# Kernel optimization log

Measured on AMD Instinct MI355X. Metric: run time of the kernel, lower is better.

Reference implementation:

```python
import jax, jax.numpy as jnp
import numpy as np

N, E, D_IN, HID = 100000, 3200000, 256, 128
EPS = 1e-5  # BatchNorm1d default eps


def batchnorm(x, gamma, beta):
    # training-mode BatchNorm1d: batch stats, biased variance
    mu = x.mean(axis=0)
    var = ((x - mu) ** 2).mean(axis=0)
    return (x - mu) * jax.lax.rsqrt(var + EPS) * gamma + beta


def setup_inputs() -> dict:
    key = jax.random.key(0)
    ks = jax.random.split(key, 6)
    s_in = 1.0 / np.sqrt(D_IN)
    s_h = 1.0 / np.sqrt(HID)
    return {
        "x": jax.random.normal(ks[0], (N, D_IN), jnp.float32),
        "edge_index": jax.random.randint(ks[1], (2, E), 0, N),
        "W1": jax.random.uniform(ks[2], (D_IN, HID), jnp.float32, -s_in, s_in),
        "b1": jnp.zeros((HID,), jnp.float32),
        "g1": jnp.ones((HID,), jnp.float32),
        "be1": jnp.zeros((HID,), jnp.float32),
        "Wl": jax.random.uniform(ks[3], (HID, HID), jnp.float32, -s_h, s_h),
        "bl": jnp.zeros((HID,), jnp.float32),
        "Wr": jax.random.uniform(ks[4], (HID, HID), jnp.float32, -s_h, s_h),
        "g2": jnp.ones((HID,), jnp.float32),
        "be2": jnp.zeros((HID,), jnp.float32),
    }


def reference(x, edge_index, W1, b1, g1, be1, Wl, bl, Wr, g2, be2):
    # input_linear: Linear -> BatchNorm1d, then ReLU
    feat = jax.nn.relu(batchnorm(x @ W1 + b1, g1, be1))  # [N, HID]

    # SAGEConv: mean-aggregate source features at destinations
    src, dst = edge_index[0], edge_index[1]
    msg_sum = jax.ops.segment_sum(feat[src], dst, num_segments=N)       # [N, HID]
    deg = jax.ops.segment_sum(jnp.ones((E, 1), feat.dtype), dst, num_segments=N)
    mean = msg_sum / jnp.maximum(deg, 1.0)

    # out = lin_l(aggr) + lin_r(x); lin_l has bias, lin_r does not (PyG default)
    out = mean @ Wl + bl + feat @ Wr
    out_feat = batchnorm(out, g2, be2)
    return feat, out_feat
```

## Files before the change

kernel.cpp:

```cpp
#include <hip/hip_runtime.h>

#define NN 100000
#define NE 3200000
#define KD 256
#define HD 128
#define NB 782
#define CAP 4608

typedef __bf16 bf16x8 __attribute__((ext_vector_type(8)));
typedef float  f32x8  __attribute__((ext_vector_type(8)));
typedef float  f32x4  __attribute__((ext_vector_type(4)));
typedef float  f32x2  __attribute__((ext_vector_type(2)));
typedef unsigned u32x2 __attribute__((ext_vector_type(2)));
typedef unsigned u32x4 __attribute__((ext_vector_type(4)));

__device__ __forceinline__ f32x4 mfma16(bf16x8 a, bf16x8 b, f32x4 c) {
  return __builtin_amdgcn_mfma_f32_16x16x32_bf16(a, b, c, 0, 0, 0);
}

__global__ void prep_w(const float* __restrict__ W1, const float* __restrict__ Wl,
                       const float* __restrict__ Wr, __bf16* __restrict__ Bt1,
                       __bf16* __restrict__ Bt2, float* __restrict__ stats,
                       int* __restrict__ bucket_cur) {
  if (blockIdx.x == 0) {
    for (int i = threadIdx.x; i < 1024; i += 256) stats[i] = 0.f;
  } else if (blockIdx.x == 1) {
    for (int i = threadIdx.x; i < NB; i += 256) bucket_cur[i] = i * CAP;
  }
  int c = blockIdx.x;
  int k = threadIdx.x;
  Bt1[c * KD + k] = (__bf16)W1[k * HD + c];
  float w = (k < HD) ? Wl[k * HD + c] : Wr[(k - HD) * HD + c];
  Bt2[c * KD + k] = (__bf16)w;
}

__global__ __launch_bounds__(1024) void b_scatter(const int* __restrict__ src,
                                                  const int* __restrict__ dst,
                                                  int* __restrict__ bucket_cur,
                                                  unsigned* __restrict__ pairs) {
  __shared__ int h[NB];
  __shared__ int cur[NB];
  __shared__ int gbase[NB];
  for (int i = threadIdx.x; i < NB; i += 1024) { h[i] = 0; cur[i] = 0; }
  __syncthreads();
  int base = blockIdx.x * 12500;
  for (int i = threadIdx.x; i < 12500; i += 1024)
    atomicAdd(&h[dst[base + i] >> 7], 1);
  __syncthreads();
  for (int b = threadIdx.x; b < NB; b += 1024) {
    int c = h[b];
    gbase[b] = c ? atomicAdd(&bucket_cur[b], c) : 0;
  }
  __syncthreads();
  for (int i = threadIdx.x; i < 12500; i += 1024) {
    int d = dst[base + i];
    int s = src[base + i];
    int b = d >> 7;
    int r = atomicAdd(&cur[b], 1);
    pairs[gbase[b] + r] = ((unsigned)s << 7) | (unsigned)(d & 127);
  }
}

__global__ __launch_bounds__(256) void b_sort(const int* __restrict__ bucket_cur,
                                              unsigned* __restrict__ pc,
                                              int* __restrict__ row_start,
                                              int* __restrict__ row_cnt) {
  __shared__ unsigned sin[CAP];
  __shared__ unsigned sout[CAP];
  __shared__ int h[128], ex[128];
  int b = blockIdx.x;
  int n0 = b * CAP;
  int cnt = bucket_cur[b] - n0;
  if (cnt > CAP) cnt = CAP;
  if (threadIdx.x < 128) h[threadIdx.x] = 0;
  __syncthreads();
  for (int i = threadIdx.x; i < cnt; i += 256) {
    unsigned v = pc[n0 + i];
    sin[i] = v;
    atomicAdd(&h[v & 127], 1);
  }
  __syncthreads();
  if (threadIdx.x < 128) ex[threadIdx.x] = h[threadIdx.x];
  __syncthreads();
  for (int off = 1; off < 128; off <<= 1) {
    int u = 0;
    if (threadIdx.x < 128 && threadIdx.x >= off) u = ex[threadIdx.x - off];
    __syncthreads();
    if (threadIdx.x < 128) ex[threadIdx.x] += u;
    __syncthreads();
  }
  if (threadIdx.x < 128) {
    int c = h[threadIdx.x];
    int excl = ex[threadIdx.x] - c;
    int node = b * 128 + threadIdx.x;
    if (node < NN) {
      row_start[node] = n0 + excl;
      row_cnt[node] = c;
    }
    h[threadIdx.x] = excl;
  }
  __syncthreads();
  for (int i = threadIdx.x; i < cnt; i += 256) {
    unsigned v = sin[i];
    int r = atomicAdd(&h[v & 127], 1);
    sout[r] = v >> 7;
  }
  __syncthreads();
  for (int i = threadIdx.x; i < cnt; i += 256)
    pc[n0 + i] = sout[i];
}

__global__ __launch_bounds__(256, 4) void gemm_x(const float* __restrict__ A,
                                                 const __bf16* __restrict__ Bt,
                                                 float* __restrict__ C,
                                                 float* __restrict__ sumc,
                                                 float* __restrict__ sqc) {
  __shared__ __bf16 sB[64 * KD];
  __shared__ float lsum[64], lsq[64];
  int tid = threadIdx.x;
  int colbase = (blockIdx.x & 1) * 64;
  int rowtile = blockIdx.x >> 1;
  if (tid < 64) { lsum[tid] = 0.f; lsq[tid] = 0.f; }
  int wave = tid >> 6, lane = tid & 63;
  int q = lane >> 4, m = lane & 15;
  int rowbase = rowtile * 256 + wave * 64;
  const float* pa[4];
#pragma unroll
  for (int g = 0; g < 4; ++g) {
    int r = rowbase + g * 16 + m;
    if (r > NN - 1) r = NN - 1;
    pa[g] = A + (size_t)r * KD + q * 8;
  }
  f32x8 u[4];
#pragma unroll
  for (int g = 0; g < 4; ++g) u[g] = *(const f32x8*)(pa[g]);
  for (int i = tid; i < 64 * KD / 8; i += 256) {
    int r = i >> 5, g = i & 31;
    bf16x8 v = *(const bf16x8*)(Bt + (size_t)(colbase + r) * KD + (g << 3));
    *(bf16x8*)(&sB[r * KD + ((g ^ (r & 7)) << 3)]) = v;
  }
  f32x4 acc[4][4];
  f32x4 z = {0.f, 0.f, 0.f, 0.f};
#pragma unroll
  for (int g = 0; g < 4; ++g)
#pragma unroll
    for (int t = 0; t < 4; ++t) acc[g][t] = z;
  __syncthreads();
#pragma unroll
  for (int k0 = 0; k0 < KD; k0 += 32) {
    bf16x8 a[4];
#pragma unroll
    for (int g = 0; g < 4; ++g) a[g] = __builtin_convertvector(u[g], bf16x8);
    if (k0 + 32 < KD) {
#pragma unroll
      for (int g = 0; g < 4; ++g) u[g] = *(const f32x8*)(pa[g] + k0 + 32);
    }
    int gb = (k0 >> 3) + q;
#pragma unroll
    for (int t = 0; t < 4; ++t) {
      int c = t * 16 + m;
      bf16x8 bb = *(const bf16x8*)(&sB[c * KD + ((gb ^ (c & 7)) << 3)]);
#pragma unroll
      for (int g = 0; g < 4; ++g) acc[g][t] = mfma16(a[g], bb, acc[g][t]);
    }
  }
  float ps[4], pq2[4];
#pragma unroll
  for (int t = 0; t < 4; ++t) { ps[t] = 0.f; pq2[t] = 0.f; }
#pragma unroll
  for (int g = 0; g < 4; ++g)
#pragma unroll
    for (int rg = 0; rg < 4; ++rg) {
      int r = rowbase + g * 16 + q * 4 + rg;
      if (r < NN) {
        float* Cr = C + (size_t)r * HD + colbase + m;
#pragma unroll
        for (int t = 0; t < 4; ++t) {
          float v = acc[g][t][rg];
          Cr[t * 16] = v;
          ps[t] += v;
          pq2[t] += v * v;
        }
      }
    }
#pragma unroll
  for (int t = 0; t < 4; ++t) {
    atomicAdd(&lsum[t * 16 + m], ps[t]);
    atomicAdd(&lsq[t * 16 + m], pq2[t]);
  }
  __syncthreads();
  if (tid < 64) {
    atomicAdd(&sumc[colbase + tid], lsum[tid]);
    atomicAdd(&sqc[colbase + tid], lsq[tid]);
  }
}

__global__ __launch_bounds__(256, 4) void gemm_cat(const __bf16* __restrict__ A0,
                                                   const __bf16* __restrict__ A1,
                                                   const __bf16* __restrict__ Bt,
                                                   float* __restrict__ C,
                                                   float* __restrict__ sumc,
                                                   float* __restrict__ sqc) {
  __shared__ __bf16 sB[64 * KD];
  __shared__ float lsum[64], lsq[64];
  int tid = threadIdx.x;
  int colbase = (blockIdx.x & 1) * 64;
  int rowtile = blockIdx.x >> 1;
  if (tid < 64) { lsum[tid] = 0.f; lsq[tid] = 0.f; }
  int wave = tid >> 6, lane = tid & 63;
  int q = lane >> 4, m = lane & 15;
  int rowbase = rowtile * 256 + wave * 64;
  const __bf16* p0[4];
  const __bf16* p1[4];
#pragma unroll
  for (int g = 0; g < 4; ++g) {
    int r = rowbase + g * 16 + m;
    if (r > NN - 1) r = NN - 1;
    p0[g] = A0 + (size_t)r * HD + q * 8;
    p1[g] = A1 + (size_t)r * HD + q * 8;
  }
  bf16x8 u[4];
#pragma unroll
  for (int g = 0; g < 4; ++g) u[g] = *(const bf16x8*)(p0[g]);
  for (int i = tid; i < 64 * KD / 8; i += 256) {
    int r = i >> 5, g = i & 31;
    bf16x8 v = *(const bf16x8*)(Bt + (size_t)(colbase + r) * KD + (g << 3));
    *(bf16x8*)(&sB[r * KD + ((g ^ (r & 7)) << 3)]) = v;
  }
  f32x4 acc[4][4];
  f32x4 z = {0.f, 0.f, 0.f, 0.f};
#pragma unroll
  for (int g = 0; g < 4; ++g)
#pragma unroll
    for (int t = 0; t < 4; ++t) acc[g][t] = z;
  __syncthreads();
#pragma unroll
  for (int k0 = 0; k0 < KD; k0 += 32) {
    bf16x8 a[4];
#pragma unroll
    for (int g = 0; g < 4; ++g) a[g] = u[g];
    int kn = k0 + 32;
    if (kn < KD) {
      int kk = kn & (HD - 1);
#pragma unroll
      for (int g = 0; g < 4; ++g)
        u[g] = (kn < HD) ? *(const bf16x8*)(p0[g] + kk)
                         : *(const bf16x8*)(p1[g] + kk);
    }
    int gb = (k0 >> 3) + q;
#pragma unroll
    for (int t = 0; t < 4; ++t) {
      int c = t * 16 + m;
      bf16x8 bb = *(const bf16x8*)(&sB[c * KD + ((gb ^ (c & 7)) << 3)]);
#pragma unroll
      for (int g = 0; g < 4; ++g) acc[g][t] = mfma16(a[g], bb, acc[g][t]);
    }
  }
  float ps[4], pq2[4];
#pragma unroll
  for (int t = 0; t < 4; ++t) { ps[t] = 0.f; pq2[t] = 0.f; }
#pragma unroll
  for (int g = 0; g < 4; ++g)
#pragma unroll
    for (int rg = 0; rg < 4; ++rg) {
      int r = rowbase + g * 16 + q * 4 + rg;
      if (r < NN) {
        float* Cr = C + (size_t)r * HD + colbase + m;
#pragma unroll
        for (int t = 0; t < 4; ++t) {
          float v = acc[g][t][rg];
          Cr[t * 16] = v;
          ps[t] += v;
          pq2[t] += v * v;
        }
      }
    }
#pragma unroll
  for (int t = 0; t < 4; ++t) {
    atomicAdd(&lsum[t * 16 + m], ps[t]);
    atomicAdd(&lsq[t * 16 + m], pq2[t]);
  }
  __syncthreads();
  if (tid < 64) {
    atomicAdd(&sumc[colbase + tid], lsum[tid]);
    atomicAdd(&sqc[colbase + tid], lsq[tid]);
  }
}

__global__ __launch_bounds__(256) void bn_apply(const float* __restrict__ X,
                                                const float* __restrict__ sumc,
                                                const float* __restrict__ sqc,
                                                const float* __restrict__ g,
                                                const float* __restrict__ be,
                                                float* __restrict__ outf,
                                                __bf16* __restrict__ outb,
                                                unsigned char* __restrict__ outq,
                                                int relu) {
  __shared__ float sc[HD], sh[HD];
  if (threadIdx.x < HD) {
    int c = threadIdx.x;
    float mu = sumc[c] * (1.0f / NN);
    float var = sqc[c] * (1.0f / NN) - mu * mu;
    float rs = rsqrtf(var + 1e-5f);
    float a = rs * g[c];
    sc[c] = a;
    sh[c] = be[c] - mu * a;
  }
  __syncthreads();
  size_t base = ((size_t)blockIdx.x * 256 + threadIdx.x) * 8;
  int c0 = (int)(base & (HD - 1));
  f32x4 x0 = *(const f32x4*)(X + base);
  f32x4 x1 = *(const f32x4*)(X + base + 4);
  float o[8];
#pragma unroll
  for (int j = 0; j < 8; ++j) {
    float xv = (j < 4) ? x0[j] : x1[j - 4];
    float v = xv * sc[c0 + j] + sh[c0 + j];
    if (relu) v = fmaxf(v, 0.f);
    o[j] = v;
  }
  f32x4 o0 = {o[0], o[1], o[2], o[3]};
  f32x4 o1 = {o[4], o[5], o[6], o[7]};
  *(f32x4*)(outf + base) = o0;
  *(f32x4*)(outf + base + 4) = o1;
  if (outb) {
    bf16x8 ob;
#pragma unroll
    for (int j = 0; j < 8; ++j) ob[j] = (__bf16)o[j];
    *(bf16x8*)(outb + base) = ob;
    int w0 = 0, w1 = 0;
    w0 = __builtin_amdgcn_cvt_pk_fp8_f32(o[0], o[1], w0, false);
    w0 = __builtin_amdgcn_cvt_pk_fp8_f32(o[2], o[3], w0, true);
    w1 = __builtin_amdgcn_cvt_pk_fp8_f32(o[4], o[5], w1, false);
    w1 = __builtin_amdgcn_cvt_pk_fp8_f32(o[6], o[7], w1, true);
    u32x2 qv = {(unsigned)w0, (unsigned)w1};
    *(u32x2*)(outq + base) = qv;
  }
}

__global__ __launch_bounds__(256) void aggregate(const int* __restrict__ row_start,
                                                 const int* __restrict__ row_cnt,
                                                 const unsigned* __restrict__ csr,
                                                 const unsigned char* __restrict__ featq,
                                                 __bf16* __restrict__ meanb) {
  int node = blockIdx.x * 4 + (threadIdx.x >> 6);
  if (node >= NN) return;
  int lane = threadIdx.x & 63;
  int sub = lane >> 3;
  int m = lane & 7;
  int s = row_start[node];
  int deg = row_cnt[node];
  int e = s + deg;
  f32x2 acc[8];
#pragma unroll
  for (int j = 0; j < 8; ++j) acc[j] = (f32x2){0.f, 0.f};
  const u32x4* rows = (const u32x4*)featq;
  for (int base = s; base < e; base += 64) {
    int nb = e - base;
    if (nb > 64) nb = 64;
    unsigned my = 0;
    if (lane < nb) my = csr[base + lane];
#pragma unroll
    for (int t = 0; t < 64; t += 8) {
      int slot = t + sub;
      unsigned sn = __shfl(my, slot, 64);
      if (slot < nb) {
        u32x4 v = rows[(size_t)sn * 8 + m];
        acc[0] += __builtin_amdgcn_cvt_pk_f32_fp8((int)v.x, false);
        acc[1] += __builtin_amdgcn_cvt_pk_f32_fp8((int)v.x, true);
        acc[2] += __builtin_amdgcn_cvt_pk_f32_fp8((int)v.y, false);
        acc[3] += __builtin_amdgcn_cvt_pk_f32_fp8((int)v.y, true);
        acc[4] += __builtin_amdgcn_cvt_pk_f32_fp8((int)v.z, false);
        acc[5] += __builtin_amdgcn_cvt_pk_f32_fp8((int)v.z, true);
        acc[6] += __builtin_amdgcn_cvt_pk_f32_fp8((int)v.w, false);
        acc[7] += __builtin_amdgcn_cvt_pk_f32_fp8((int)v.w, true);
      }
    }
  }
#pragma unroll
  for (int j = 0; j < 8; ++j) {
    acc[j].x += __shfl_xor(acc[j].x, 8, 64);
    acc[j].y += __shfl_xor(acc[j].y, 8, 64);
    acc[j].x += __shfl_xor(acc[j].x, 16, 64);
    acc[j].y += __shfl_xor(acc[j].y, 16, 64);
    acc[j].x += __shfl_xor(acc[j].x, 32, 64);
    acc[j].y += __shfl_xor(acc[j].y, 32, 64);
  }
  if (sub == 0) {
    float inv = 1.0f / (float)(deg < 1 ? 1 : deg);
    bf16x8 o0, o1;
#pragma unroll
    for (int j = 0; j < 4; ++j) {
      o0[2 * j]     = (__bf16)(acc[j].x * inv);
      o0[2 * j + 1] = (__bf16)(acc[j].y * inv);
      o1[2 * j]     = (__bf16)(acc[4 + j].x * inv);
      o1[2 * j + 1] = (__bf16)(acc[4 + j].y * inv);
    }
    __bf16* dst = meanb + (size_t)node * HD + m * 16;
    *(bf16x8*)dst = o0;
    *(bf16x8*)(dst + 8) = o1;
  }
}

extern "C" void kernel_launch(void* const* d_in, const int* in_sizes, int n_in,
                              void* d_out, int out_size, void* d_ws, size_t ws_size,
                              hipStream_t stream) {
  (void)in_sizes; (void)n_in; (void)out_size; (void)ws_size;
  const float* x   = (const float*)d_in[0];
  const int*   ei  = (const int*)d_in[1];
  const float* W1  = (const float*)d_in[2];
  const float* g1  = (const float*)d_in[4];
  const float* be1 = (const float*)d_in[5];
  const float* Wl  = (const float*)d_in[6];
  const float* Wr  = (const float*)d_in[8];
  const float* g2  = (const float*)d_in[9];
  const float* be2 = (const float*)d_in[10];

  float* feat_out = (float*)d_out;
  float* out_feat = feat_out + (size_t)NN * HD;
  unsigned char* featq = (unsigned char*)out_feat;

  char* w = (char*)d_ws;
  float*    h          = (float*)(w);
  __bf16*   featb      = (__bf16*)(w + 51200000);
  __bf16*   meanb      = (__bf16*)(w + 76800000);
  unsigned* pc         = (unsigned*)(w + 102400000);
  int*      row_start  = (int*)(w + 116814848);
  int*      row_cnt    = (int*)(w + 117214848);
  int*      bucket_cur = (int*)(w + 117614848);
  float*    stats      = (float*)(w + 117618944);
  __bf16*   Bt1        = (__bf16*)(w + 117623040);
  __bf16*   Bt2        = (__bf16*)(w + 117688576);

  float* sum1 = stats,       * sq1 = stats + 128;
  float* sum2 = stats + 512, * sq2 = stats + 640;

  const int* esrc = ei;
  const int* edst = ei + NE;

  prep_w<<<128, 256, 0, stream>>>(W1, Wl, Wr, Bt1, Bt2, stats, bucket_cur);
  b_scatter<<<256, 1024, 0, stream>>>(esrc, edst, bucket_cur, pc);
  b_sort<<<NB, 256, 0, stream>>>(bucket_cur, pc, row_start, row_cnt);

  gemm_x<<<782, 256, 0, stream>>>(x, Bt1, h, sum1, sq1);
  bn_apply<<<6250, 256, 0, stream>>>(h, sum1, sq1, g1, be1, feat_out, featb, featq, 1);

  aggregate<<<25000, 256, 0, stream>>>(row_start, row_cnt, pc, featq, meanb);

  gemm_cat<<<782, 256, 0, stream>>>(meanb, featb, Bt2, h, sum2, sq2);
  bn_apply<<<6250, 256, 0, stream>>>(h, sum2, sq2, g2, be2, out_feat,
                                     (__bf16*)nullptr, (unsigned char*)nullptr, 0);
}
```

Before: 449.5 us.

## Compute full 128-column output per block to read A rows once

```diff
diff --git a/kernel.cpp b/kernel.cpp
--- a/kernel.cpp
+++ b/kernel.cpp
@@ -110,180 +110,166 @@
     pc[n0 + i] = sout[i];
 }
 
-__global__ __launch_bounds__(256, 4) void gemm_x(const float* __restrict__ A,
+__global__ __launch_bounds__(256, 2) void gemm_x(const float* __restrict__ A,
                                                  const __bf16* __restrict__ Bt,
                                                  float* __restrict__ C,
                                                  float* __restrict__ sumc,
                                                  float* __restrict__ sqc) {
-  __shared__ __bf16 sB[64 * KD];
-  __shared__ float lsum[64], lsq[64];
+  __shared__ __bf16 sB[HD * KD];
+  __shared__ float lsum[HD], lsq[HD];
   int tid = threadIdx.x;
-  int colbase = (blockIdx.x & 1) * 64;
-  int rowtile = blockIdx.x >> 1;
-  if (tid < 64) { lsum[tid] = 0.f; lsq[tid] = 0.f; }
+  if (tid < HD) { lsum[tid] = 0.f; lsq[tid] = 0.f; }
   int wave = tid >> 6, lane = tid & 63;
   int q = lane >> 4, m = lane & 15;
-  int rowbase = rowtile * 256 + wave * 64;
-  const float* pa[4];
+  int rowbase = blockIdx.x * 256 + wave * 64;
+  for (int i = tid; i < HD * KD / 8; i += 256) {
+    int r = i >> 5, g = i & 31;
+    bf16x8 v = *(const bf16x8*)(Bt + (size_t)r * KD + (g << 3));
+    *(bf16x8*)(&sB[r * KD + ((g ^ (r & 7)) << 3)]) = v;
+  }
+  bf16x8 areg[4][8];
 #pragma unroll
   for (int g = 0; g < 4; ++g) {
     int r = rowbase + g * 16 + m;
     if (r > NN - 1) r = NN - 1;
-    pa[g] = A + (size_t)r * KD + q * 8;
-  }
-  f32x8 u[4];
-#pragma unroll
-  for (int g = 0; g < 4; ++g) u[g] = *(const f32x8*)(pa[g]);
-  for (int i = tid; i < 64 * KD / 8; i += 256) {
-    int r = i >> 5, g = i & 31;
-    bf16x8 v = *(const bf16x8*)(Bt + (size_t)(colbase + r) * KD + (g << 3));
-    *(bf16x8*)(&sB[r * KD + ((g ^ (r & 7)) << 3)]) = v;
-  }
-  f32x4 acc[4][4];
-  f32x4 z = {0.f, 0.f, 0.f, 0.f};
-#pragma unroll
-  for (int g = 0; g < 4; ++g)
-#pragma unroll
-    for (int t = 0; t < 4; ++t) acc[g][t] = z;
-  __syncthreads();
-#pragma unroll
-  for (int k0 = 0; k0 < KD; k0 += 32) {
-    bf16x8 a[4];
-#pragma unroll
-    for (int g = 0; g < 4; ++g) a[g] = __builtin_convertvector(u[g], bf16x8);
-    if (k0 + 32 < KD) {
-#pragma unroll
-      for (int g = 0; g < 4; ++g) u[g] = *(const f32x8*)(pa[g] + k0 + 32);
-    }
-    int gb = (k0 >> 3) + q;
-#pragma unroll
-    for (int t = 0; t < 4; ++t) {
-      int c = t * 16 + m;
-      bf16x8 bb = *(const bf16x8*)(&sB[c * KD + ((gb ^ (c & 7)) << 3)]);
-#pragma unroll
-      for (int g = 0; g < 4; ++g) acc[g][t] = mfma16(a[g], bb, acc[g][t]);
-    }
-  }
-  float ps[4], pq2[4];
-#pragma unroll
-  for (int t = 0; t < 4; ++t) { ps[t] = 0.f; pq2[t] = 0.f; }
-#pragma unroll
-  for (int g = 0; g < 4; ++g)
-#pragma unroll
-    for (int rg = 0; rg < 4; ++rg) {
-      int r = rowbase + g * 16 + q * 4 + rg;
-      if (r < NN) {
-        float* Cr = C + (size_t)r * HD + colbase + m;
-#pragma unroll
-        for (int t = 0; t < 4; ++t) {
-          float v = acc[g][t][rg];
-          Cr[t * 16] = v;
-          ps[t] += v;
-          pq2[t] += v * v;
+    const float* pa = A + (size_t)r * KD + q * 8;
+    f32x8 u[8];
+#pragma unroll
+    for (int k = 0; k < 8; ++k) u[k] = *(const f32x8*)(pa + k * 32);
+#pragma unroll
+    for (int k = 0; k < 8; ++k) areg[g][k] = __builtin_convertvector(u[k], bf16x8);
+  }
+  __syncthreads();
+#pragma unroll
+  for (int hh = 0; hh < 2; ++hh) {
+    f32x4 acc[4][4];
+    f32x4 z = {0.f, 0.f, 0.f, 0.f};
+#pragma unroll
+    for (int g = 0; g < 4; ++g)
+#pragma unroll
+      for (int t = 0; t < 4; ++t) acc[g][t] = z;
+#pragma unroll
+    for (int ks = 0; ks < 8; ++ks) {
+      int gb = ks * 4 + q;
+#pragma unroll
+      for (int t = 0; t < 4; ++t) {
+        int c = hh * 64 + t * 16 + m;
+        bf16x8 bb = *(const bf16x8*)(&sB[c * KD + ((gb ^ (c & 7)) << 3)]);
+#pragma unroll
+        for (int g = 0; g < 4; ++g) acc[g][t] = mfma16(areg[g][ks], bb, acc[g][t]);
+      }
+    }
+    float ps[4], pq2[4];
+#pragma unroll
+    for (int t = 0; t < 4; ++t) { ps[t] = 0.f; pq2[t] = 0.f; }
+#pragma unroll
+    for (int g = 0; g < 4; ++g)
+#pragma unroll
+      for (int rg = 0; rg < 4; ++rg) {
+        int r = rowbase + g * 16 + q * 4 + rg;
+        if (r < NN) {
+          float* Cr = C + (size_t)r * HD + hh * 64 + m;
+#pragma unroll
+          for (int t = 0; t < 4; ++t) {
+            float v = acc[g][t][rg];
+            Cr[t * 16] = v;
+            ps[t] += v;
+            pq2[t] += v * v;
+          }
         }
       }
-    }
-#pragma unroll
-  for (int t = 0; t < 4; ++t) {
-    atomicAdd(&lsum[t * 16 + m], ps[t]);
-    atomicAdd(&lsq[t * 16 + m], pq2[t]);
-  }
-  __syncthreads();
-  if (tid < 64) {
-    atomicAdd(&sumc[colbase + tid], lsum[tid]);
-    atomicAdd(&sqc[colbase + tid], lsq[tid]);
-  }
-}
-
-__global__ __launch_bounds__(256, 4) void gemm_cat(const __bf16* __restrict__ A0,
+#pragma unroll
+    for (int t = 0; t < 4; ++t) {
+      atomicAdd(&lsum[hh * 64 + t * 16 + m], ps[t]);
+      atomicAdd(&lsq[hh * 64 + t * 16 + m], pq2[t]);
+    }
+  }
+  __syncthreads();
+  if (tid < HD) {
+    atomicAdd(&sumc[tid], lsum[tid]);
+    atomicAdd(&sqc[tid], lsq[tid]);
+  }
+}
+
+__global__ __launch_bounds__(256, 2) void gemm_cat(const __bf16* __restrict__ A0,
                                                    const __bf16* __restrict__ A1,
                                                    const __bf16* __restrict__ Bt,
                                                    float* __restrict__ C,
                                                    float* __restrict__ sumc,
                                                    float* __restrict__ sqc) {
-  __shared__ __bf16 sB[64 * KD];
-  __shared__ float lsum[64], lsq[64];
+  __shared__ __bf16 sB[HD * KD];
+  __shared__ float lsum[HD], lsq[HD];
   int tid = threadIdx.x;
-  int colbase = (blockIdx.x & 1) * 64;
-  int rowtile = blockIdx.x >> 1;
-  if (tid < 64) { lsum[tid] = 0.f; lsq[tid] = 0.f; }
+  if (tid < HD) { lsum[tid] = 0.f; lsq[tid] = 0.f; }
   int wave = tid >> 6, lane = tid & 63;
   int q = lane >> 4, m = lane & 15;
-  int rowbase = rowtile * 256 + wave * 64;
-  const __bf16* p0[4];
-  const __bf16* p1[4];
+  int rowbase = blockIdx.x * 256 + wave * 64;
+  for (int i = tid; i < HD * KD / 8; i += 256) {
+    int r = i >> 5, g = i & 31;
+    bf16x8 v = *(const bf16x8*)(Bt + (size_t)r * KD + (g << 3));
+    *(bf16x8*)(&sB[r * KD + ((g ^ (r & 7)) << 3)]) = v;
+  }
+  bf16x8 areg[4][8];
 #pragma unroll
   for (int g = 0; g < 4; ++g) {
     int r = rowbase + g * 16 + m;
     if (r > NN - 1) r = NN - 1;
-    p0[g] = A0 + (size_t)r * HD + q * 8;
-    p1[g] = A1 + (size_t)r * HD + q * 8;
-  }
-  bf16x8 u[4];
-#pragma unroll
-  for (int g = 0; g < 4; ++g) u[g] = *(const bf16x8*)(p0[g]);
-  for (int i = tid; i < 64 * KD / 8; i += 256) {
-    int r = i >> 5, g = i & 31;
-    bf16x8 v = *(const bf16x8*)(Bt + (size_t)(colbase + r) * KD + (g << 3));
-    *(bf16x8*)(&sB[r * KD + ((g ^ (r & 7)) << 3)]) = v;
-  }
-  f32x4 acc[4][4];
-  f32x4 z = {0.f, 0.f, 0.f, 0.f};
-#pragma unroll
-  for (int g = 0; g < 4; ++g)
-#pragma unroll
-    for (int t = 0; t < 4; ++t) acc[g][t] = z;
-  __syncthreads();
-#pragma unroll
-  for (int k0 = 0; k0 < KD; k0 += 32) {
-    bf16x8 a[4];
-#pragma unroll
-    for (int g = 0; g < 4; ++g) a[g] = u[g];
-    int kn = k0 + 32;
-    if (kn < KD) {
-      int kk = kn & (HD - 1);
-#pragma unroll
-      for (int g = 0; g < 4; ++g)
-        u[g] = (kn < HD) ? *(const bf16x8*)(p0[g] + kk)
-                         : *(const bf16x8*)(p1[g] + kk);
-    }
-    int gb = (k0 >> 3) + q;
-#pragma unroll
-    for (int t = 0; t < 4; ++t) {
-      int c = t * 16 + m;
-      bf16x8 bb = *(const bf16x8*)(&sB[c * KD + ((gb ^ (c & 7)) << 3)]);
-#pragma unroll
-      for (int g = 0; g < 4; ++g) acc[g][t] = mfma16(a[g], bb, acc[g][t]);
-    }
-  }
-  float ps[4], pq2[4];
-#pragma unroll
-  for (int t = 0; t < 4; ++t) { ps[t] = 0.f; pq2[t] = 0.f; }
-#pragma unroll
-  for (int g = 0; g < 4; ++g)
-#pragma unroll
-    for (int rg = 0; rg < 4; ++rg) {
-      int r = rowbase + g * 16 + q * 4 + rg;
-      if (r < NN) {
-        float* Cr = C + (size_t)r * HD + colbase + m;
-#pragma unroll
-        for (int t = 0; t < 4; ++t) {
-          float v = acc[g][t][rg];
-          Cr[t * 16] = v;
-          ps[t] += v;
-          pq2[t] += v * v;
+    const __bf16* p0 = A0 + (size_t)r * HD + q * 8;
+    const __bf16* p1 = A1 + (size_t)r * HD + q * 8;
+#pragma unroll
+    for (int k = 0; k < 4; ++k) areg[g][k] = *(const bf16x8*)(p0 + k * 32);
+#pragma unroll
+    for (int k = 0; k < 4; ++k) areg[g][4 + k] = *(const bf16x8*)(p1 + k * 32);
+  }
+  __syncthreads();
+#pragma unroll
+  for (int hh = 0; hh < 2; ++hh) {
+    f32x4 acc[4][4];
+    f32x4 z = {0.f, 0.f, 0.f, 0.f};
+#pragma unroll
+    for (int g = 0; g < 4; ++g)
+#pragma unroll
+      for (int t = 0; t < 4; ++t) acc[g][t] = z;
+#pragma unroll
+    for (int ks = 0; ks < 8; ++ks) {
+      int gb = ks * 4 + q;
+#pragma unroll
+      for (int t = 0; t < 4; ++t) {
+        int c = hh * 64 + t * 16 + m;
+        bf16x8 bb = *(const bf16x8*)(&sB[c * KD + ((gb ^ (c & 7)) << 3)]);
+#pragma unroll
+        for (int g = 0; g < 4; ++g) acc[g][t] = mfma16(areg[g][ks], bb, acc[g][t]);
+      }
+    }
+    float ps[4], pq2[4];
+#pragma unroll
+    for (int t = 0; t < 4; ++t) { ps[t] = 0.f; pq2[t] = 0.f; }
+#pragma unroll
+    for (int g = 0; g < 4; ++g)
+#pragma unroll
+      for (int rg = 0; rg < 4; ++rg) {
+        int r = rowbase + g * 16 + q * 4 + rg;
+        if (r < NN) {
+          float* Cr = C + (size_t)r * HD + hh * 64 + m;
+#pragma unroll
+          for (int t = 0; t < 4; ++t) {
+            float v = acc[g][t][rg];
+            Cr[t * 16] = v;
+            ps[t] += v;
+            pq2[t] += v * v;
+          }
         }
       }
-    }
-#pragma unroll
-  for (int t = 0; t < 4; ++t) {
-    atomicAdd(&lsum[t * 16 + m], ps[t]);
-    atomicAdd(&lsq[t * 16 + m], pq2[t]);
-  }
-  __syncthreads();
-  if (tid < 64) {
-    atomicAdd(&sumc[colbase + tid], lsum[tid]);
-    atomicAdd(&sqc[colbase + tid], lsq[tid]);
+#pragma unroll
+    for (int t = 0; t < 4; ++t) {
+      atomicAdd(&lsum[hh * 64 + t * 16 + m], ps[t]);
+      atomicAdd(&lsq[hh * 64 + t * 16 + m], pq2[t]);
+    }
+  }
+  __syncthreads();
+  if (tid < HD) {
+    atomicAdd(&sumc[tid], lsum[tid]);
+    atomicAdd(&sqc[tid], lsq[tid]);
   }
 }
 
@@ -442,12 +428,12 @@
   b_scatter<<<256, 1024, 0, stream>>>(esrc, edst, bucket_cur, pc);
   b_sort<<<NB, 256, 0, stream>>>(bucket_cur, pc, row_start, row_cnt);
 
-  gemm_x<<<782, 256, 0, stream>>>(x, Bt1, h, sum1, sq1);
+  gemm_x<<<391, 256, 0, stream>>>(x, Bt1, h, sum1, sq1);
   bn_apply<<<6250, 256, 0, stream>>>(h, sum1, sq1, g1, be1, feat_out, featb, featq, 1);
 
   aggregate<<<25000, 256, 0, stream>>>(row_start, row_cnt, pc, featq, meanb);
 
-  gemm_cat<<<782, 256, 0, stream>>>(meanb, featb, Bt2, h, sum2, sq2);
+  gemm_cat<<<391, 256, 0, stream>>>(meanb, featb, Bt2, h, sum2, sq2);
   bn_apply<<<6250, 256, 0, stream>>>(h, sum2, sq2, g2, be2, out_feat,
                                      (__bf16*)nullptr, (unsigned char*)nullptr, 0);
 }
```

Result: faster. 435.1 us (-3.2%).
